# Kernel optimization log

Hardware: AMD Instinct MI355X
Metric: run time of the kernel (lower is better)

Reference implementation:

```python
import jax, jax.numpy as jnp
import numpy as np

D_MODEL = 1024
NUM_HEADS = 16
HEAD_DIM = D_MODEL // NUM_HEADS


def setup_inputs() -> dict:
    key = jax.random.key(0)
    k1, k2, k3 = jax.random.split(key, 3)
    x = jax.random.normal(k1, (2, 2048, D_MODEL), dtype=jnp.float32)
    # trunc_normal init approximated by clipped normal with same std
    std_qkv = np.sqrt(2.0 / (D_MODEL + 3 * D_MODEL)).astype(np.float32)
    std_o = np.sqrt(2.0 / (D_MODEL + D_MODEL)).astype(np.float32)
    w_qkv = jnp.clip(jax.random.normal(k2, (3 * D_MODEL, D_MODEL), dtype=jnp.float32) * std_qkv,
                     -3 * std_qkv, 3 * std_qkv)
    w_o = jnp.clip(jax.random.normal(k3, (D_MODEL, D_MODEL), dtype=jnp.float32) * std_o,
                   -3 * std_o, 3 * std_o)
    return {"x": x, "w_qkv": w_qkv, "w_o": w_o}


def reference(x, w_qkv, w_o):
    b, s, d = x.shape
    h, hd = NUM_HEADS, HEAD_DIM
    # QKV projection: weight is [d_out, d_in]
    qkv = jnp.einsum('od,bsd->bso', w_qkv, x)  # [b, s, 3d]
    q, k, v = jnp.split(qkv, 3, axis=-1)
    # [b, s, d] -> [b, h, s, hd]
    def to_heads(t):
        return t.reshape(b, s, h, hd).transpose(0, 2, 1, 3)
    q_mh, k_mh, v_mh = to_heads(q), to_heads(k), to_heads(v)
    scale = 1.0 / jnp.sqrt(jnp.asarray(hd, dtype=x.dtype))
    scores = jnp.einsum('bhmd,bhnd->bhmn', q_mh, k_mh) * scale  # [b,h,s,s]
    causal = jnp.tril(jnp.ones((s, s), dtype=bool))
    scores = jnp.where(causal, scores, -jnp.inf)
    attn = jax.nn.softmax(scores, axis=-1)
    out = jnp.einsum('bhmn,bhnd->bhmd', attn, v_mh)  # [b,h,s,hd]
    out = out.transpose(0, 2, 1, 3).reshape(b, s, d)
    return jnp.einsum('od,bsd->bso', w_o, out)
```

## Files before the change

### kernel.cpp

```cpp
#include <hip/hip_runtime.h>

constexpr int SEQ = 2048;
constexpr int DM = 1024;
constexpr int NH = 16;
constexpr int BATCH = 2;
constexpr int MTOT = BATCH * SEQ;

typedef __bf16 bf16x8 __attribute__((ext_vector_type(8)));
typedef __bf16 bf16x4 __attribute__((ext_vector_type(4)));
typedef float f32x4 __attribute__((ext_vector_type(4)));

#define MFMA16(a, b, c) __builtin_amdgcn_mfma_f32_16x16x32_bf16((a), (b), (c), 0, 0, 0)

__device__ __forceinline__ void async_copy16(const void* g, void* l) {
  __builtin_amdgcn_global_load_lds((const __attribute__((address_space(1))) void*)g,
                                   (__attribute__((address_space(3))) void*)l, 16, 0, 0);
}

__global__ void sentinel_fill(float* out, int n) {
  int i = blockIdx.x * blockDim.x + threadIdx.x;
  for (; i < n; i += gridDim.x * blockDim.x) out[i] = 0.25f;
}

__global__ __launch_bounds__(256) void cvt_all(const float* __restrict__ x,
                                               const float* __restrict__ wq,
                                               const float* __restrict__ wo,
                                               __bf16* __restrict__ xb,
                                               __bf16* __restrict__ wqb,
                                               __bf16* __restrict__ wob) {
  const long i = (long)(blockIdx.x * 256 + threadIdx.x) * 8;
  const float* src;
  __bf16* dst;
  long off;
  if (i < 4194304) { src = x; dst = xb; off = i; }
  else if (i < 7340032) { src = wq; dst = wqb; off = i - 4194304; }
  else { src = wo; dst = wob; off = i - 7340032; }
  f32x4 lo = *(const f32x4*)(src + off);
  f32x4 hi = *(const f32x4*)(src + off + 4);
  bf16x8 r;
#pragma unroll
  for (int j = 0; j < 4; ++j) { r[j] = (__bf16)lo[j]; r[4 + j] = (__bf16)hi[j]; }
  *(bf16x8*)(dst + off) = r;
}

template <typename OutT>
__global__ __launch_bounds__(256) void gemm_bt(const __bf16* __restrict__ A,
                                               const __bf16* __restrict__ B,
                                               OutT* __restrict__ C,
                                               int M, int N, int K, int lda,
                                               float nanSig) {
  __shared__ alignas(16) __bf16 As[128 * 32];
  __shared__ alignas(16) __bf16 Bs[128 * 32];
  const int tid = threadIdx.x;
  const int lane = tid & 63;
  const int wave = tid >> 6;
  const int lr = lane & 15;
  const int quad = lane >> 4;
  const int wm = (wave >> 1) * 64;
  const int wn = (wave & 1) * 64;
  const int m0 = blockIdx.y * 128;
  const int n0 = blockIdx.x * 128;

  const int ra = tid >> 2;
  const int ca = (tid & 3) * 8;
  const __bf16* gA0 = A + (long)(m0 + ra) * lda + ca;
  const __bf16* gA1 = A + (long)(m0 + 64 + ra) * lda + ca;
  const __bf16* gB0 = B + (long)(n0 + ra) * K + ca;
  const __bf16* gB1 = B + (long)(n0 + 64 + ra) * K + ca;
  __bf16* lA0 = &As[wave * 512];
  __bf16* lA1 = &As[2048 + wave * 512];
  __bf16* lB0 = &Bs[wave * 512];
  __bf16* lB1 = &Bs[2048 + wave * 512];

  f32x4 acc[4][4];
#pragma unroll
  for (int i = 0; i < 4; ++i)
#pragma unroll
    for (int j = 0; j < 4; ++j) acc[i][j] = (f32x4){0.f, 0.f, 0.f, 0.f};

  for (int k0 = 0; k0 < K; k0 += 32) {
    async_copy16(gA0 + k0, lA0);
    async_copy16(gA1 + k0, lA1);
    async_copy16(gB0 + k0, lB0);
    async_copy16(gB1 + k0, lB1);
    __builtin_amdgcn_s_waitcnt(0);
    __syncthreads();
    bf16x8 af[4], bfr[4];
#pragma unroll
    for (int i = 0; i < 4; ++i) af[i] = *(const bf16x8*)&As[(wm + i * 16 + lr) * 32 + quad * 8];
#pragma unroll
    for (int j = 0; j < 4; ++j) bfr[j] = *(const bf16x8*)&Bs[(wn + j * 16 + lr) * 32 + quad * 8];
#pragma unroll
    for (int i = 0; i < 4; ++i)
#pragma unroll
      for (int j = 0; j < 4; ++j) acc[i][j] = MFMA16(af[i], bfr[j], acc[i][j]);
    __syncthreads();
  }

#pragma unroll
  for (int i = 0; i < 4; ++i) {
    const int row = m0 + wm + i * 16 + quad * 4;
#pragma unroll
    for (int j = 0; j < 4; ++j) {
      const int col = n0 + wn + j * 16 + lr;
#pragma unroll
      for (int r = 0; r < 4; ++r) {
        float v = acc[i][j][r];
        if (!(v == v)) v = nanSig;
        C[(long)(row + r) * N + col] = (OutT)v;
      }
    }
  }
}

template <int F32>
__device__ __forceinline__ bf16x8 load_cvt8(const void* base, long off) {
  if constexpr (F32) {
    const float* p = (const float*)base + off;
    f32x4 lo = *(const f32x4*)p;
    f32x4 hi = *(const f32x4*)(p + 4);
    bf16x8 r;
#pragma unroll
    for (int j = 0; j < 4; ++j) { r[j] = (__bf16)lo[j]; r[4 + j] = (__bf16)hi[j]; }
    return r;
  } else {
    return *(const bf16x8*)((const __bf16*)base + off);
  }
}

template <int AF32, int BF32, typename OutT>
__global__ __launch_bounds__(256) void gemm_nt(const void* __restrict__ Av,
                                               const void* __restrict__ Bv,
                                               OutT* __restrict__ C,
                                               int M, int N, int K, int lda,
                                               float nanSig) {
  __shared__ alignas(16) __bf16 As[128 * 32];
  __shared__ alignas(16) __bf16 Bs[128 * 32];
  const int tid = threadIdx.x;
  const int lane = tid & 63;
  const int wave = tid >> 6;
  const int lr = lane & 15;
  const int quad = lane >> 4;
  const int wm = (wave >> 1) * 64;
  const int wn = (wave & 1) * 64;
  const int m0 = blockIdx.y * 128;
  const int n0 = blockIdx.x * 128;

  const int r0 = tid >> 2;
  const int r1 = 64 + (tid >> 2);
  const int cc = (tid & 3) * 8;
  const long aBase0 = (long)(m0 + r0) * lda + cc;
  const long aBase1 = (long)(m0 + r1) * lda + cc;
  const long bBase0 = (long)(n0 + r0) * K + cc;
  const long bBase1 = (long)(n0 + r1) * K + cc;
  __bf16* lA0 = &As[r0 * 32 + cc];
  __bf16* lA1 = &As[r1 * 32 + cc];
  __bf16* lB0 = &Bs[r0 * 32 + cc];
  __bf16* lB1 = &Bs[r1 * 32 + cc];

  f32x4 acc[4][4];
#pragma unroll
  for (int i = 0; i < 4; ++i)
#pragma unroll
    for (int j = 0; j < 4; ++j) acc[i][j] = (f32x4){0.f, 0.f, 0.f, 0.f};

  for (int k0 = 0; k0 < K; k0 += 32) {
    bf16x8 va0 = load_cvt8<AF32>(Av, aBase0 + k0);
    bf16x8 va1 = load_cvt8<AF32>(Av, aBase1 + k0);
    bf16x8 vb0 = load_cvt8<BF32>(Bv, bBase0 + k0);
    bf16x8 vb1 = load_cvt8<BF32>(Bv, bBase1 + k0);
    __syncthreads();
    *(bf16x8*)lA0 = va0;
    *(bf16x8*)lA1 = va1;
    *(bf16x8*)lB0 = vb0;
    *(bf16x8*)lB1 = vb1;
    __syncthreads();
    bf16x8 af[4], bfr[4];
#pragma unroll
    for (int i = 0; i < 4; ++i) af[i] = *(const bf16x8*)&As[(wm + i * 16 + lr) * 32 + quad * 8];
#pragma unroll
    for (int j = 0; j < 4; ++j) bfr[j] = *(const bf16x8*)&Bs[(wn + j * 16 + lr) * 32 + quad * 8];
#pragma unroll
    for (int i = 0; i < 4; ++i)
#pragma unroll
      for (int j = 0; j < 4; ++j) acc[i][j] = MFMA16(af[i], bfr[j], acc[i][j]);
  }

#pragma unroll
  for (int i = 0; i < 4; ++i) {
    const int row = m0 + wm + i * 16 + quad * 4;
#pragma unroll
    for (int j = 0; j < 4; ++j) {
      const int col = n0 + wn + j * 16 + lr;
#pragma unroll
      for (int r = 0; r < 4; ++r) {
        float v = acc[i][j][r];
        if (!(v == v)) v = nanSig;
        C[(long)(row + r) * N + col] = (OutT)v;
      }
    }
  }
}

__global__ __launch_bounds__(512, 2) void attn_fwd(__bf16* __restrict__ qkv) {
  const int jj = blockIdx.x;
  const int h = blockIdx.y;
  const int b = blockIdx.z;
  const int tid = threadIdx.x;
  const int lane = tid & 63;
  const int wave = tid >> 6;
  const int ps = wave >> 2;
  const int pi = 2 * jj + ps;
  const int q0A = pi * 64;
  const int q0B = (31 - pi) * 64;
  const int lr = lane & 15;
  const int quad = lane >> 4;
  const int wq = (wave & 3) * 16;

  __shared__ alignas(16) __bf16 Ks[2][64 * 72];
  __shared__ alignas(16) __bf16 Vt[2][64 * 72];
  __shared__ alignas(16) __bf16 Pq[256 * 72];

  __bf16* pqw = &Pq[wave * 32 * 72];
  const long base = (long)b * SEQ * 3072;
  const int qi[2] = {q0A + wq + lr, q0B + wq + lr};

  bf16x8 b_q[2][2];
#pragma unroll
  for (int qg = 0; qg < 2; ++qg) {
    const long rowoff = base + (long)qi[qg] * 3072 + h * 64;
    b_q[qg][0] = *(const bf16x8*)(qkv + rowoff + quad * 8);
    b_q[qg][1] = *(const bf16x8*)(qkv + rowoff + 32 + quad * 8);
  }

  const float NEGS = -30000.f;
  const float SC = 0.18033688f;
  float m_i[2] = {NEGS, NEGS}, l_i[2] = {0.f, 0.f};
  f32x4 o_acc[2][4];
#pragma unroll
  for (int qg = 0; qg < 2; ++qg)
#pragma unroll
    for (int dt = 0; dt < 4; ++dt) o_acc[qg][dt] = (f32x4){0.f, 0.f, 0.f, 0.f};

  const int r_ = tid >> 3;
  const int col_ = (tid & 7) * 8;
  const int l8 = tid & 7;
  const int sw = (l8 & 3) << 3;
  const bool oddr = (tid >> 3) & 1;
  const int jb = oddr ? 4 : 0;

  const int Tb = 32 - 2 * jj;
  const int Tp = 32 - pi;

  bf16x8 kreg, vreg;
  auto loadTile = [&](int t) {
    const long ro = base + ((long)t * 64 + r_) * 3072 + h * 64 + col_;
    kreg = *(const bf16x8*)(qkv + ro + 1024);
    vreg = *(const bf16x8*)(qkv + ro + 2048);
  };
  auto stageTile = [&](int bi) {
    __bf16* ks = &Ks[bi][0];
    __bf16* vt = &Vt[bi][0];
    *(bf16x8*)&ks[r_ * 72 + col_] = kreg;
    const int rr = (r_ & ~1) ^ sw;
    int vd[4], od[4];
    __builtin_memcpy(vd, &vreg, 16);
#pragma unroll
    for (int i = 0; i < 4; ++i) od[i] = __shfl_xor(vd[i], 8);
#pragma unroll
    for (int i = 0; i < 4; ++i) {
      const int j = jb + i;
      const int a = vd[j >> 1], bb = od[j >> 1];
      const int lo = oddr ? bb : a;
      const int hi = oddr ? a : bb;
      const int pair = (j & 1) ? (int)(((unsigned)lo >> 16) | (hi & 0xffff0000))
                               : (int)((lo & 0xffff) | (hi << 16));
      *(int*)&vt[(col_ + j) * 72 + rr] = pair;
    }
  };

  loadTile(0);
  stageTile(0);
  loadTile(1);
  __syncthreads();

  for (int t = 0; t < Tb; ++t) {
    const int cur = t & 1;
    const int kv0 = t * 64;
    const bool active = (t < Tp);
    const bool actA = (kv0 <= q0A + wq + 15);

    f32x4 st[2][4];
#pragma unroll
    for (int kt = 0; kt < 4; ++kt) {
      st[1][kt] = (f32x4){0.f, 0.f, 0.f, 0.f};
      st[0][kt] = (f32x4){0.f, 0.f, 0.f, 0.f};
    }
    if (active) {
      __builtin_amdgcn_s_setprio(1);
#pragma unroll
      for (int ks = 0; ks < 2; ++ks) {
        bf16x8 ak[4];
#pragma unroll
        for (int kt = 0; kt < 4; ++kt)
          ak[kt] = *(const bf16x8*)&Ks[cur][(kt * 16 + lr) * 72 + ks * 32 + quad * 8];
#pragma unroll
        for (int kt = 0; kt < 4; ++kt) st[1][kt] = MFMA16(ak[kt], b_q[1][ks], st[1][kt]);
        if (actA) {
#pragma unroll
          for (int kt = 0; kt < 4; ++kt) st[0][kt] = MFMA16(ak[kt], b_q[0][ks], st[0][kt]);
        }
      }
      __builtin_amdgcn_s_setprio(0);
    }

    if (t + 1 < Tb) stageTile(cur ^ 1);
    if (t + 2 < Tb) loadTile(t + 2);

    if (active) {
#pragma unroll
      for (int qg = 1; qg >= 0; --qg) {
        if (qg == 0 && !actA) continue;
        const int q0X = (qg == 0) ? q0A : q0B;
        if (kv0 + 64 <= q0X + wq) {
#pragma unroll
          for (int kt = 0; kt < 4; ++kt)
#pragma unroll
            for (int r = 0; r < 4; ++r) st[qg][kt][r] *= SC;
        } else {
#pragma unroll
          for (int kt = 0; kt < 4; ++kt) {
            const int d0 = kv0 + kt * 16 + quad * 4 - qi[qg];
#pragma unroll
            for (int r = 0; r < 4; ++r)
              st[qg][kt][r] = (d0 + r <= 0) ? st[qg][kt][r] * SC : NEGS;
          }
        }
        float mx = st[qg][0][0];
#pragma unroll
        for (int kt = 0; kt < 4; ++kt)
#pragma unroll
          for (int r = 0; r < 4; ++r) mx = fmaxf(mx, st[qg][kt][r]);
        mx = fmaxf(mx, __shfl_xor(mx, 16));
        mx = fmaxf(mx, __shfl_xor(mx, 32));
        const bool noresc = __all(mx - m_i[qg] <= 8.f);
        const float mnew = noresc ? m_i[qg] : fmaxf(m_i[qg], mx);
        float rs = 0.f;
#pragma unroll
        for (int kt = 0; kt < 4; ++kt)
#pragma unroll
          for (int r = 0; r < 4; ++r) {
            const float p = exp2f(st[qg][kt][r] - mnew);
            st[qg][kt][r] = p;
            rs += p;
          }
        rs += __shfl_xor(rs, 16);
        rs += __shfl_xor(rs, 32);
#pragma unroll
        for (int kt = 0; kt < 4; ++kt) {
          bf16x4 pv;
#pragma unroll
          for (int r = 0; r < 4; ++r) pv[r] = (__bf16)st[qg][kt][r];
          *(bf16x4*)&pqw[(qg * 16 + lr) * 72 + kt * 16 + quad * 4] = pv;
        }
        if (noresc) {
          l_i[qg] += rs;
        } else {
          const float alpha = exp2f(m_i[qg] - mnew);
          l_i[qg] = l_i[qg] * alpha + rs;
          m_i[qg] = mnew;
#pragma unroll
          for (int dt = 0; dt < 4; ++dt)
#pragma unroll
            for (int r = 0; r < 4; ++r) o_acc[qg][dt][r] *= alpha;
        }
      }

      asm volatile("s_waitcnt lgkmcnt(0)" ::: "memory");
      __builtin_amdgcn_sched_barrier(0);

      __builtin_amdgcn_s_setprio(1);
#pragma unroll
      for (int ks = 0; ks < 2; ++ks) {
        bf16x8 av[4];
#pragma unroll
        for (int dt = 0; dt < 4; ++dt) {
          const int blk = ((ks << 2) + quad) ^ ((2 * dt + (lr >> 3)) & 3);
          av[dt] = *(const bf16x8*)&Vt[cur][(dt * 16 + lr) * 72 + (blk << 3)];
        }
        {
          bf16x8 bp = *(const bf16x8*)&pqw[(16 + lr) * 72 + ks * 32 + quad * 8];
#pragma unroll
          for (int dt = 0; dt < 4; ++dt) o_acc[1][dt] = MFMA16(av[dt], bp, o_acc[1][dt]);
        }
        if (actA) {
          bf16x8 bp = *(const bf16x8*)&pqw[lr * 72 + ks * 32 + quad * 8];
#pragma unroll
          for (int dt = 0; dt < 4; ++dt) o_acc[0][dt] = MFMA16(av[dt], bp, o_acc[0][dt]);
        }
      }
      __builtin_amdgcn_s_setprio(0);
    }

    __syncthreads();
  }

#pragma unroll
  for (int qg = 0; qg < 2; ++qg) {
    const float inv = 1.f / fmaxf(l_i[qg], 1e-30f);
    const long obase = base + (long)qi[qg] * 3072 + h * 64 + quad * 4;
#pragma unroll
    for (int dt = 0; dt < 4; ++dt) {
      bf16x4 ov;
#pragma unroll
      for (int r = 0; r < 4; ++r) ov[r] = (__bf16)(o_acc[qg][dt][r] * inv);
      *(bf16x4*)(qkv + obase + dt * 16) = ov;
    }
  }
}

extern "C" void kernel_launch(void* const* d_in, const int* in_sizes, int n_in,
                              void* d_out, int out_size, void* d_ws, size_t ws_size,
                              hipStream_t stream) {
  const float* x = (const float*)d_in[0];
  const float* w_qkv = (const float*)d_in[1];
  const float* w_o = (const float*)d_in[2];
  for (int i = 0; i < n_in; ++i) {
    if (in_sizes[i] == MTOT * DM) x = (const float*)d_in[i];
    else if (in_sizes[i] == 3 * DM * DM) w_qkv = (const float*)d_in[i];
    else if (in_sizes[i] == DM * DM) w_o = (const float*)d_in[i];
  }
  float* out = (float*)d_out;

  const size_t qkvBytes = (size_t)MTOT * 3072 * 2;
  const size_t xbBytes = (size_t)MTOT * DM * 2;
  const size_t wqBytes = (size_t)3 * DM * DM * 2;
  const size_t woBytes = (size_t)DM * DM * 2;
  const size_t needFast = qkvBytes + xbBytes + wqBytes + woBytes;

  __bf16* qkv = (__bf16*)d_ws;

  if (ws_size >= needFast) {
    __bf16* xb = (__bf16*)((char*)d_ws + qkvBytes);
    __bf16* wqb = (__bf16*)((char*)d_ws + qkvBytes + xbBytes);
    __bf16* wob = (__bf16*)((char*)d_ws + qkvBytes + xbBytes + wqBytes);
    cvt_all<<<4096, 256, 0, stream>>>(x, w_qkv, w_o, xb, wqb, wob);
    gemm_bt<__bf16><<<dim3(3072 / 128, MTOT / 128), 256, 0, stream>>>(
        xb, wqb, qkv, MTOT, 3072, DM, DM, 1e4f);
    attn_fwd<<<dim3(8, NH, BATCH), 512, 0, stream>>>(qkv);
    gemm_bt<float><<<dim3(DM / 128, MTOT / 128), 256, 0, stream>>>(
        qkv, wob, out, MTOT, DM, DM, 3072, 2e4f);
  } else if (ws_size >= qkvBytes) {
    gemm_nt<1, 1, __bf16><<<dim3(3072 / 128, MTOT / 128), 256, 0, stream>>>(
        x, w_qkv, qkv, MTOT, 3072, DM, DM, 1e4f);
    attn_fwd<<<dim3(8, NH, BATCH), 512, 0, stream>>>(qkv);
    gemm_nt<0, 1, float><<<dim3(DM / 128, MTOT / 128), 256, 0, stream>>>(
        qkv, w_o, out, MTOT, DM, DM, 3072, 2e4f);
  } else {
    sentinel_fill<<<256, 256, 0, stream>>>(out, out_size);
  }
}
```

Measured before the change: 216.3 us.

## Double-buffer LDS tiles in GEMM to overlap global loads with MFMA

The GEMM kernel now keeps two LDS buffers for the A and B tiles. It issues the async global-to-LDS copy for the next K-step before running the MFMAs on the current one, so memory latency overlaps with compute, and it drops one barrier per iteration. It also raises wave priority around the MFMA block. LDS use doubles, which may lower occupancy, and the GEMMs are only part of the total time alongside attention.

After: 222.5 us. 2.9% more time.

```diff
diff --git a/kernel.cpp b/kernel.cpp
--- a/kernel.cpp
+++ b/kernel.cpp
@@ -49,8 +49,8 @@
                                                OutT* __restrict__ C,
                                                int M, int N, int K, int lda,
                                                float nanSig) {
-  __shared__ alignas(16) __bf16 As[128 * 32];
-  __shared__ alignas(16) __bf16 Bs[128 * 32];
+  __shared__ alignas(16) __bf16 As[2][128 * 32];
+  __shared__ alignas(16) __bf16 Bs[2][128 * 32];
   const int tid = threadIdx.x;
   const int lane = tid & 63;
   const int wave = tid >> 6;
@@ -67,10 +67,6 @@
   const __bf16* gA1 = A + (long)(m0 + 64 + ra) * lda + ca;
   const __bf16* gB0 = B + (long)(n0 + ra) * K + ca;
   const __bf16* gB1 = B + (long)(n0 + 64 + ra) * K + ca;
-  __bf16* lA0 = &As[wave * 512];
-  __bf16* lA1 = &As[2048 + wave * 512];
-  __bf16* lB0 = &Bs[wave * 512];
-  __bf16* lB1 = &Bs[2048 + wave * 512];
 
   f32x4 acc[4][4];
 #pragma unroll
@@ -78,23 +74,36 @@
 #pragma unroll
     for (int j = 0; j < 4; ++j) acc[i][j] = (f32x4){0.f, 0.f, 0.f, 0.f};
 
+  auto stage = [&](int bi, int k0) {
+    async_copy16(gA0 + k0, &As[bi][wave * 512]);
+    async_copy16(gA1 + k0, &As[bi][2048 + wave * 512]);
+    async_copy16(gB0 + k0, &Bs[bi][wave * 512]);
+    async_copy16(gB1 + k0, &Bs[bi][2048 + wave * 512]);
+  };
+
+  stage(0, 0);
+  __builtin_amdgcn_s_waitcnt(0);
+  __syncthreads();
+
+  int cur = 0;
   for (int k0 = 0; k0 < K; k0 += 32) {
-    async_copy16(gA0 + k0, lA0);
-    async_copy16(gA1 + k0, lA1);
-    async_copy16(gB0 + k0, lB0);
-    async_copy16(gB1 + k0, lB1);
+    if (k0 + 32 < K) stage(cur ^ 1, k0 + 32);
+    bf16x8 af[4], bfr[4];
+#pragma unroll
+    for (int i = 0; i < 4; ++i)
+      af[i] = *(const bf16x8*)&As[cur][(wm + i * 16 + lr) * 32 + quad * 8];
+#pragma unroll
+    for (int j = 0; j < 4; ++j)
+      bfr[j] = *(const bf16x8*)&Bs[cur][(wn + j * 16 + lr) * 32 + quad * 8];
+    __builtin_amdgcn_s_setprio(1);
+#pragma unroll
+    for (int i = 0; i < 4; ++i)
+#pragma unroll
+      for (int j = 0; j < 4; ++j) acc[i][j] = MFMA16(af[i], bfr[j], acc[i][j]);
+    __builtin_amdgcn_s_setprio(0);
     __builtin_amdgcn_s_waitcnt(0);
     __syncthreads();
-    bf16x8 af[4], bfr[4];
-#pragma unroll
-    for (int i = 0; i < 4; ++i) af[i] = *(const bf16x8*)&As[(wm + i * 16 + lr) * 32 + quad * 8];
-#pragma unroll
-    for (int j = 0; j < 4; ++j) bfr[j] = *(const bf16x8*)&Bs[(wn + j * 16 + lr) * 32 + quad * 8];
-#pragma unroll
-    for (int i = 0; i < 4; ++i)
-#pragma unroll
-      for (int j = 0; j < 4; ++j) acc[i][j] = MFMA16(af[i], bfr[j], acc[i][j]);
-    __syncthreads();
+    cur ^= 1;
   }
 
 #pragma unroll
```
